# Optimization experiments

Measured on AMD Instinct MI355X. Metric: run time of the kernel, lower is better.

The kernel has to match this reference:

```python
import jax, jax.numpy as jnp
import numpy as np

B, T, D = 4, 2048, 1024
H = 16
DH = D // H
BASE = 10000.0


def _rope_tables(seq_len, dim):
    inv_freq = 1.0 / (BASE ** (np.arange(0, dim, 2, dtype=np.float32) / dim))
    pos = np.arange(seq_len, dtype=np.float32)
    freqs = np.outer(pos, inv_freq)            # (T, dim/2)
    emb = np.concatenate([freqs, freqs], -1)   # (T, dim)
    return jnp.asarray(np.cos(emb)), jnp.asarray(np.sin(emb))


def setup_inputs() -> dict:
    key = jax.random.key(0)
    ks = jax.random.split(key, 5)
    s = 1.0 / np.sqrt(D)
    x = jax.random.normal(ks[0], (B, T, D), jnp.float32)
    Wqkv = jax.random.normal(ks[1], (D, 3 * D), jnp.float32) * s
    bqkv = jnp.zeros((3 * D,), jnp.float32)
    Wproj = jax.random.normal(ks[2], (D, D), jnp.float32) * s
    bproj = jnp.zeros((D,), jnp.float32)
    cos, sin = _rope_tables(T, DH)
    return {"x": x, "Wqkv": Wqkv, "bqkv": bqkv, "Wproj": Wproj,
            "bproj": bproj, "cos": cos, "sin": sin}


def _rotate_half(u):
    u1, u2 = jnp.split(u, 2, axis=-1)
    return jnp.concatenate([-u2, u1], axis=-1)


def reference(x, Wqkv, bqkv, Wproj, bproj, cos, sin):
    b, t, d = x.shape
    qkv = x @ Wqkv + bqkv                       # (B, T, 3D)
    qkv = qkv.reshape(b, t, 3, H, DH)           # matches '(three h d)' order
    q, k, v = qkv[:, :, 0], qkv[:, :, 1], qkv[:, :, 2]  # (B, T, H, DH)
    c = cos[None, :, None, :]                   # (1, T, 1, DH)
    s = sin[None, :, None, :]
    q = q * c + _rotate_half(q) * s
    k = k * c + _rotate_half(k) * s
    scale = DH ** -0.5
    attn = jnp.einsum('bthd,bshd->bhts', q, k) * scale   # (B, H, T, T)
    attn = jax.nn.softmax(attn, axis=-1)
    out = jnp.einsum('bhts,bshd->bthd', attn, v)          # (B, T, H, DH)
    out = out.reshape(b, t, d)
    return out @ Wproj + bproj
```

## Files before the change

kernel.cpp:

```cpp
#include <hip/hip_runtime.h>


typedef _Float16 half_t;
typedef _Float16 half8 __attribute__((ext_vector_type(8)));
typedef _Float16 half4v __attribute__((ext_vector_type(4)));
typedef __fp16 fp16x2 __attribute__((ext_vector_type(2)));
typedef float floatx4 __attribute__((ext_vector_type(4)));

#define MFMA_F16 __builtin_amdgcn_mfma_f32_16x16x32_f16

constexpr int Bdim = 4, T = 2048, D = 1024, H = 16, DH = 64;
constexpr int Mrows = Bdim * T;
constexpr int N1 = 3 * D;
constexpr int KD = D;
constexpr int NT = KD / 32;

constexpr float QSCALE = 0.125f * 1.4426950408889634f;
constexpr float CSHIFT = 4.0f * 1.4426950408889634f;

__device__ __forceinline__ void gl_lds16(const half_t* g, half_t* l) {
  __builtin_amdgcn_global_load_lds(
      (const __attribute__((address_space(1))) void*)g,
      (__attribute__((address_space(3))) void*)l, 16, 0, 0);
}

__global__ __launch_bounds__(256) void cvt_kernel(const float* __restrict__ s,
                                                  half_t* __restrict__ d, int n4) {
  int i = blockIdx.x * 256 + threadIdx.x;
  if (i < n4) {
    float4 v = ((const float4*)s)[i];
    half4v h;
    h[0] = (half_t)v.x; h[1] = (half_t)v.y; h[2] = (half_t)v.z; h[3] = (half_t)v.w;
    ((half4v*)d)[i] = h;
  }
}

__global__ __launch_bounds__(64) void cvt_transpose(const float* __restrict__ W,
                                                    half_t* __restrict__ Wt,
                                                    int Kr, int Nc) {
  __shared__ half_t Th[32][36];
  const int l = threadIdx.x;
  const int n0 = blockIdx.x * 32, k0 = blockIdx.y * 32;
#pragma unroll
  for (int i = 0; i < 4; ++i) {
    int kk = (l >> 3) + i * 8;
    int nn4 = (l & 7) * 4;
    float4 v = *(const float4*)(W + (size_t)(k0 + kk) * Nc + n0 + nn4);
    half4v h;
    h[0] = (half_t)v.x; h[1] = (half_t)v.y; h[2] = (half_t)v.z; h[3] = (half_t)v.w;
    *(half4v*)&Th[kk][nn4] = h;
  }
  __syncthreads();
#pragma unroll
  for (int i = 0; i < 4; ++i) {
    int nn = (l >> 3) + i * 8;
    int kk4 = (l & 7) * 4;
    half4v h;
#pragma unroll
    for (int j = 0; j < 4; ++j) h[j] = Th[kk4 + j][nn];
    *(half4v*)(Wt + (size_t)(n0 + nn) * Kr + k0 + kk4) = h;
  }
}

__global__ __launch_bounds__(256, 3) void gemm_qkv_rope(
    const half_t* __restrict__ X, const half_t* __restrict__ Wt,
    const float* __restrict__ bias, const float* __restrict__ cosT,
    const float* __restrict__ sinT,
    half_t* __restrict__ Q, half_t* __restrict__ K, half_t* __restrict__ V) {
  __shared__ half_t As[3 * 128 * 32];
  __shared__ half_t Bs[3 * 128 * 32];
  const int tid = threadIdx.x;
  const int lane = tid & 63, wv = tid >> 6;
  const int wm = wv >> 1, wn = wv & 1;
  const int qd = lane >> 4, ln = lane & 15;
  const int flat = blockIdx.y * 24 + blockIdx.x;
  const int swzb = (flat & 7) * 192 + (flat >> 3);
  const int bn = swzb % 24, bm = swzb / 24;

  floatx4 acc[4][4] = {};

#pragma unroll
  for (int pt = 0; pt < 2; ++pt) {
#pragma unroll
    for (int p = 0; p < 2; ++p) {
      int c = tid + p * 256;
      int row = c >> 2, col = (c & 3) << 3;
      gl_lds16(X + (size_t)(bm * 128 + row) * KD + pt * 32 + col, As + pt * 4096 + c * 8);
      gl_lds16(Wt + (size_t)(bn * 128 + row) * KD + pt * 32 + col, Bs + pt * 4096 + c * 8);
    }
  }
  asm volatile("s_waitcnt vmcnt(4)" ::: "memory");
  __builtin_amdgcn_s_barrier();

  int rd = 0, st = 2;
  for (int t = 0; t < NT; ++t) {
    if (t + 2 < NT) {
#pragma unroll
      for (int p = 0; p < 2; ++p) {
        int c = tid + p * 256;
        int row = c >> 2, col = (c & 3) << 3;
        gl_lds16(X + (size_t)(bm * 128 + row) * KD + (t + 2) * 32 + col, As + st * 4096 + c * 8);
        gl_lds16(Wt + (size_t)(bn * 128 + row) * KD + (t + 2) * 32 + col, Bs + st * 4096 + c * 8);
      }
    }
    const half_t* Ab = As + rd * 4096;
    const half_t* Bb = Bs + rd * 4096;
    half8 af[4], bf[4];
#pragma unroll
    for (int mi = 0; mi < 4; ++mi)
      af[mi] = *(const half8*)&Ab[(wm * 64 + mi * 16 + ln) * 32 + qd * 8];
#pragma unroll
    for (int ni = 0; ni < 4; ++ni)
      bf[ni] = *(const half8*)&Bb[(wn * 64 + ni * 16 + ln) * 32 + qd * 8];
    __builtin_amdgcn_s_setprio(1);
#pragma unroll
    for (int mi = 0; mi < 4; ++mi)
#pragma unroll
      for (int ni = 0; ni < 4; ++ni)
        acc[mi][ni] = MFMA_F16(af[mi], bf[ni], acc[mi][ni], 0, 0, 0);
    __builtin_amdgcn_s_setprio(0);
    if (t + 2 < NT) asm volatile("s_waitcnt vmcnt(4)" ::: "memory");
    else            asm volatile("s_waitcnt vmcnt(0)" ::: "memory");
    __builtin_amdgcn_s_barrier();
    rd = (rd == 2) ? 0 : rd + 1;
    st = (st == 2) ? 0 : st + 1;
  }

  const int n0 = bn * 128 + wn * 64;
  const int sreg = n0 >> 10;
  const int h = (n0 & 1023) >> 6;
  float bv[4];
#pragma unroll
  for (int ni = 0; ni < 4; ++ni) bv[ni] = bias[n0 + ni * 16 + ln];

  if (sreg == 2) {
#pragma unroll
    for (int mi = 0; mi < 4; ++mi) {
      int m0 = bm * 128 + wm * 64 + mi * 16 + qd * 4;
      int b = m0 >> 11, t0 = m0 & (T - 1);
#pragma unroll
      for (int ni = 0; ni < 4; ++ni) {
        int dh = ni * 16 + ln;
        half4v hv;
#pragma unroll
        for (int r = 0; r < 4; ++r) hv[r] = (half_t)(acc[mi][ni][r] + bv[ni]);
        *(half4v*)(V + ((size_t)(b * H + h) * DH + dh) * T + t0) = hv;
      }
    }
  } else {
    const float qscale = (sreg == 0) ? QSCALE : 1.0f;
    half_t* OUT = (sreg == 0) ? Q : K;
#pragma unroll
    for (int mi = 0; mi < 4; ++mi) {
#pragma unroll
      for (int r = 0; r < 4; ++r) {
        int m = bm * 128 + wm * 64 + mi * 16 + qd * 4 + r;
        int b = m >> 11, t = m & (T - 1);
        float v0 = acc[mi][0][r] + bv[0];
        float v1 = acc[mi][1][r] + bv[1];
        float v2 = acc[mi][2][r] + bv[2];
        float v3 = acc[mi][3][r] + bv[3];
        float c0 = cosT[t * 64 + ln],      s0 = sinT[t * 64 + ln];
        float c1 = cosT[t * 64 + 16 + ln], s1 = sinT[t * 64 + 16 + ln];
        float c2 = cosT[t * 64 + 32 + ln], s2 = sinT[t * 64 + 32 + ln];
        float c3 = cosT[t * 64 + 48 + ln], s3 = sinT[t * 64 + 48 + ln];
        float o0 = v0 * c0 - v2 * s0;
        float o1 = v1 * c1 - v3 * s1;
        float o2 = v2 * c2 + v0 * s2;
        float o3 = v3 * c3 + v1 * s3;
        size_t base = ((size_t)(b * H + h) * T + t) * DH;
        OUT[base + 0 * 16 + ln] = (half_t)(o0 * qscale);
        OUT[base + 1 * 16 + ln] = (half_t)(o1 * qscale);
        OUT[base + 2 * 16 + ln] = (half_t)(o2 * qscale);
        OUT[base + 3 * 16 + ln] = (half_t)(o3 * qscale);
      }
    }
  }
}

__global__ __launch_bounds__(512, 4) void flash_attn(
    const half_t* __restrict__ Q, const half_t* __restrict__ K,
    const half_t* __restrict__ Vt, half_t* __restrict__ AO) {
  __shared__ __align__(16) half_t Klds[2][64 * 64];
  __shared__ __align__(16) half_t Vlds[2][64 * 64];
  __shared__ __align__(16) half_t Pw[8][32 * 64];
  const int tid = threadIdx.x;
  const int lane = tid & 63, wv = tid >> 6;
  const int qd = lane >> 4, ln = lane & 15;
  const int flat = blockIdx.y * 8 + blockIdx.x;
  const int swzb = (flat & 7) * 64 + (flat >> 3);
  const int bh = swzb >> 3;
  const int q0 = (swzb & 7) * 256 + wv * 32;
  const half_t* Qb = Q + (size_t)bh * T * DH;
  const half_t* Kb = K + (size_t)bh * T * DH;
  const half_t* Vb = Vt + (size_t)bh * DH * T;
  half_t* Pq = Pw[wv];
  const int swz = (ln & 7) << 3;
  const fp16x2 one2 = {(__fp16)1.0f, (__fp16)1.0f};

  const int sr = tid >> 3, sc8 = (tid & 7) << 3;
  const int stoff = sr * 64 + (sc8 ^ ((sr & 7) << 3));
  const half_t* Kg = Kb + (size_t)sr * DH + sc8;
  const half_t* Vg = Vb + (size_t)sr * T + sc8;

  half8 qf[2][2];
#pragma unroll
  for (int mi = 0; mi < 2; ++mi)
#pragma unroll
    for (int ks = 0; ks < 2; ++ks)
      qf[mi][ks] = *(const half8*)(Qb + (size_t)(q0 + mi * 16 + ln) * DH + ks * 32 + qd * 8);

  floatx4 Oacc[2][4] = {};
  float La[2] = {0.f, 0.f};
  float Lb2[2] = {0.f, 0.f};

  half8 kreg = *(const half8*)Kg;
  half8 vreg = *(const half8*)Vg;
  *(half8*)&Klds[0][stoff] = kreg;
  *(half8*)&Vlds[0][stoff] = vreg;
  kreg = *(const half8*)(Kg + (size_t)64 * DH);
  vreg = *(const half8*)(Vg + 64);

  for (int t = 0; t < T / 64; ++t) {
    __syncthreads();
    if (t + 1 < T / 64) {
      *(half8*)&Klds[(t + 1) & 1][stoff] = kreg;
      *(half8*)&Vlds[(t + 1) & 1][stoff] = vreg;
      if (t + 2 < T / 64) {
        kreg = *(const half8*)(Kg + (size_t)(t + 2) * 64 * DH);
        vreg = *(const half8*)(Vg + (t + 2) * 64);
      }
    }
    const half_t* Kc = Klds[t & 1];
    const half_t* Vc = Vlds[t & 1];

#pragma unroll
    for (int ni = 0; ni < 4; ++ni) {
      floatx4 s4[2] = {floatx4{-CSHIFT, -CSHIFT, -CSHIFT, -CSHIFT},
                       floatx4{-CSHIFT, -CSHIFT, -CSHIFT, -CSHIFT}};
#pragma unroll
      for (int ks = 0; ks < 2; ++ks) {
        int krow = ni * 16 + ln;
        half8 kf = *(const half8*)&Kc[krow * 64 + (((ks * 32) | (qd * 8)) ^ swz)];
        __builtin_amdgcn_s_setprio(1);
#pragma unroll
        for (int mi = 0; mi < 2; ++mi)
          s4[mi] = MFMA_F16(kf, qf[mi][ks], s4[mi], 0, 0, 0);
        __builtin_amdgcn_s_setprio(0);
      }
#pragma unroll
      for (int mi = 0; mi < 2; ++mi) {
        float p0 = __builtin_amdgcn_exp2f(s4[mi][0]);
        float p1 = __builtin_amdgcn_exp2f(s4[mi][1]);
        float p2 = __builtin_amdgcn_exp2f(s4[mi][2]);
        float p3 = __builtin_amdgcn_exp2f(s4[mi][3]);
        fp16x2 h01 = __builtin_amdgcn_cvt_pkrtz(p0, p1);
        fp16x2 h23 = __builtin_amdgcn_cvt_pkrtz(p2, p3);
        La[mi]  = __builtin_amdgcn_fdot2(h01, one2, La[mi], false);
        Lb2[mi] = __builtin_amdgcn_fdot2(h23, one2, Lb2[mi], false);
        union { half4v h4; fp16x2 h2[2]; } pu;
        pu.h2[0] = h01; pu.h2[1] = h23;
        int row = mi * 16 + ln;
        int chunk = ni * 16 + ((qd >> 1) << 3);
        int low = (qd & 1) << 2;
        *(half4v*)&Pq[row * 64 + (chunk ^ swz) + low] = pu.h4;
      }
    }

#pragma unroll
    for (int ks = 0; ks < 2; ++ks) {
      half8 pf[2];
#pragma unroll
      for (int mi = 0; mi < 2; ++mi)
        pf[mi] = *(const half8*)&Pq[(mi * 16 + ln) * 64 + (((ks * 32) | (qd * 8)) ^ swz)];
#pragma unroll
      for (int di = 0; di < 4; ++di) {
        half8 vf = *(const half8*)&Vc[(di * 16 + ln) * 64 + (((ks * 32) | (qd * 8)) ^ swz)];
        __builtin_amdgcn_s_setprio(1);
#pragma unroll
        for (int mi = 0; mi < 2; ++mi)
          Oacc[mi][di] = MFMA_F16(pf[mi], vf, Oacc[mi][di], 0, 0, 0);
        __builtin_amdgcn_s_setprio(0);
      }
    }
  }

  float Ls[2];
#pragma unroll
  for (int mi = 0; mi < 2; ++mi) {
    Ls[mi] = La[mi] + Lb2[mi];
    Ls[mi] += __shfl_xor(Ls[mi], 16);
    Ls[mi] += __shfl_xor(Ls[mi], 32);
  }

  const int b = bh >> 4, h = bh & 15;
#pragma unroll
  for (int mi = 0; mi < 2; ++mi) {
#pragma unroll
    for (int r = 0; r < 4; ++r) {
      float invL = 1.f / __shfl(Ls[mi], qd * 4 + r);
      int t = q0 + mi * 16 + qd * 4 + r;
      size_t base = ((size_t)b * T + t) * D + h * DH;
#pragma unroll
      for (int di = 0; di < 4; ++di)
        AO[base + di * 16 + ln] = (half_t)(Oacc[mi][di][r] * invL);
    }
  }
}

__global__ __launch_bounds__(256, 3) void gemm_proj(
    const half_t* __restrict__ X, const half_t* __restrict__ Wt,
    const float* __restrict__ bias, float* __restrict__ OUTF) {
  __shared__ half_t As[3 * 128 * 32];
  __shared__ half_t Bs[3 * 128 * 32];
  const int tid = threadIdx.x;
  const int lane = tid & 63, wv = tid >> 6;
  const int wm = wv >> 1, wn = wv & 1;
  const int qd = lane >> 4, ln = lane & 15;
  const int flat = blockIdx.y * 8 + blockIdx.x;
  const int swzb = (flat & 7) * 64 + (flat >> 3);
  const int bn = swzb % 8, bm = swzb / 8;

  floatx4 acc[4][4] = {};

#pragma unroll
  for (int pt = 0; pt < 2; ++pt) {
#pragma unroll
    for (int p = 0; p < 2; ++p) {
      int c = tid + p * 256;
      int row = c >> 2, col = (c & 3) << 3;
      gl_lds16(X + (size_t)(bm * 128 + row) * KD + pt * 32 + col, As + pt * 4096 + c * 8);
      gl_lds16(Wt + (size_t)(bn * 128 + row) * KD + pt * 32 + col, Bs + pt * 4096 + c * 8);
    }
  }
  asm volatile("s_waitcnt vmcnt(4)" ::: "memory");
  __builtin_amdgcn_s_barrier();

  int rd = 0, st = 2;
  for (int t = 0; t < NT; ++t) {
    if (t + 2 < NT) {
#pragma unroll
      for (int p = 0; p < 2; ++p) {
        int c = tid + p * 256;
        int row = c >> 2, col = (c & 3) << 3;
        gl_lds16(X + (size_t)(bm * 128 + row) * KD + (t + 2) * 32 + col, As + st * 4096 + c * 8);
        gl_lds16(Wt + (size_t)(bn * 128 + row) * KD + (t + 2) * 32 + col, Bs + st * 4096 + c * 8);
      }
    }
    const half_t* Ab = As + rd * 4096;
    const half_t* Bb = Bs + rd * 4096;
    half8 af[4], bf[4];
#pragma unroll
    for (int mi = 0; mi < 4; ++mi)
      af[mi] = *(const half8*)&Ab[(wm * 64 + mi * 16 + ln) * 32 + qd * 8];
#pragma unroll
    for (int ni = 0; ni < 4; ++ni)
      bf[ni] = *(const half8*)&Bb[(wn * 64 + ni * 16 + ln) * 32 + qd * 8];
    __builtin_amdgcn_s_setprio(1);
#pragma unroll
    for (int mi = 0; mi < 4; ++mi)
#pragma unroll
      for (int ni = 0; ni < 4; ++ni)
        acc[mi][ni] = MFMA_F16(af[mi], bf[ni], acc[mi][ni], 0, 0, 0);
    __builtin_amdgcn_s_setprio(0);
    if (t + 2 < NT) asm volatile("s_waitcnt vmcnt(4)" ::: "memory");
    else            asm volatile("s_waitcnt vmcnt(0)" ::: "memory");
    __builtin_amdgcn_s_barrier();
    rd = (rd == 2) ? 0 : rd + 1;
    st = (st == 2) ? 0 : st + 1;
  }

  const int n0 = bn * 128 + wn * 64;
  float bv[4];
#pragma unroll
  for (int ni = 0; ni < 4; ++ni) bv[ni] = bias[n0 + ni * 16 + ln];
#pragma unroll
  for (int mi = 0; mi < 4; ++mi) {
#pragma unroll
    for (int r = 0; r < 4; ++r) {
      int m = bm * 128 + wm * 64 + mi * 16 + qd * 4 + r;
#pragma unroll
      for (int ni = 0; ni < 4; ++ni)
        OUTF[(size_t)m * D + n0 + ni * 16 + ln] = acc[mi][ni][r] + bv[ni];
    }
  }
}

extern "C" void kernel_launch(void* const* d_in, const int* in_sizes, int n_in,
                              void* d_out, int out_size, void* d_ws, size_t ws_size,
                              hipStream_t stream) {
  const float* x     = (const float*)d_in[0];
  const float* Wqkv  = (const float*)d_in[1];
  const float* bqkv  = (const float*)d_in[2];
  const float* Wproj = (const float*)d_in[3];
  const float* bproj = (const float*)d_in[4];
  const float* cosT  = (const float*)d_in[5];
  const float* sinT  = (const float*)d_in[6];
  float* out = (float*)d_out;

  half_t* xh      = (half_t*)d_ws;
  half_t* Wqkvt   = xh + (size_t)Mrows * KD;
  half_t* Wprojt  = Wqkvt + (size_t)KD * N1;
  half_t* Qb      = Wprojt + (size_t)D * D;
  half_t* Kb      = Qb + (size_t)Bdim * H * T * DH;
  half_t* Vb      = Kb + (size_t)Bdim * H * T * DH;
  half_t* AO      = xh;

  cvt_kernel<<<(Mrows * KD / 4 + 255) / 256, 256, 0, stream>>>(x, xh, Mrows * KD / 4);
  cvt_transpose<<<dim3(N1 / 32, KD / 32), 64, 0, stream>>>(Wqkv, Wqkvt, KD, N1);
  cvt_transpose<<<dim3(D / 32, KD / 32), 64, 0, stream>>>(Wproj, Wprojt, KD, D);

  gemm_qkv_rope<<<dim3(N1 / 128, Mrows / 128), 256, 0, stream>>>(
      xh, Wqkvt, bqkv, cosT, sinT, Qb, Kb, Vb);
  flash_attn<<<dim3(T / 256, Bdim * H), 512, 0, stream>>>(Qb, Kb, Vb, AO);
  gemm_proj<<<dim3(D / 128, Mrows / 128), 256, 0, stream>>>(AO, Wprojt, bproj, out);
}
```

Measured before the change: 280.0 us.

## Fuse prep conversions into one kernel and deepen flash-attn K/V pipeline

```diff
diff --git a/kernel.cpp b/kernel.cpp
--- a/kernel.cpp
+++ b/kernel.cpp
@@ -24,23 +24,10 @@
       (__attribute__((address_space(3))) void*)l, 16, 0, 0);
 }
 
-__global__ __launch_bounds__(256) void cvt_kernel(const float* __restrict__ s,
-                                                  half_t* __restrict__ d, int n4) {
-  int i = blockIdx.x * 256 + threadIdx.x;
-  if (i < n4) {
-    float4 v = ((const float4*)s)[i];
-    half4v h;
-    h[0] = (half_t)v.x; h[1] = (half_t)v.y; h[2] = (half_t)v.z; h[3] = (half_t)v.w;
-    ((half4v*)d)[i] = h;
-  }
-}
-
-__global__ __launch_bounds__(64) void cvt_transpose(const float* __restrict__ W,
-                                                    half_t* __restrict__ Wt,
-                                                    int Kr, int Nc) {
-  __shared__ half_t Th[32][36];
-  const int l = threadIdx.x;
-  const int n0 = blockIdx.x * 32, k0 = blockIdx.y * 32;
+__device__ __forceinline__ void transpose_tile32(const float* __restrict__ W,
+                                                 half_t* __restrict__ Wt,
+                                                 int Kr, int Nc, int n0, int k0,
+                                                 int l, half_t (*Th)[36]) {
 #pragma unroll
   for (int i = 0; i < 4; ++i) {
     int kk = (l >> 3) + i * 8;
@@ -59,6 +46,29 @@
 #pragma unroll
     for (int j = 0; j < 4; ++j) h[j] = Th[kk4 + j][nn];
     *(half4v*)(Wt + (size_t)(n0 + nn) * Kr + k0 + kk4) = h;
+  }
+}
+
+__global__ __launch_bounds__(256) void prep_kernel(
+    const float* __restrict__ x, half_t* __restrict__ xh,
+    const float* __restrict__ Wqkv, half_t* __restrict__ Wqkvt,
+    const float* __restrict__ Wproj, half_t* __restrict__ Wprojt) {
+  __shared__ half_t Th[4][32][36];
+  const int bid = blockIdx.x, tid = threadIdx.x;
+  if (bid < 8192) {
+    int i = bid * 256 + tid;
+    float4 v = ((const float4*)x)[i];
+    half4v h;
+    h[0] = (half_t)v.x; h[1] = (half_t)v.y; h[2] = (half_t)v.z; h[3] = (half_t)v.w;
+    ((half4v*)xh)[i] = h;
+  } else if (bid < 8192 + 768) {
+    int tile = (bid - 8192) * 4 + (tid >> 6);
+    int n0 = (tile % 96) * 32, k0 = (tile / 96) * 32;
+    transpose_tile32(Wqkv, Wqkvt, KD, N1, n0, k0, tid & 63, Th[tid >> 6]);
+  } else {
+    int tile = (bid - 8960) * 4 + (tid >> 6);
+    int n0 = (tile % 32) * 32, k0 = (tile / 32) * 32;
+    transpose_tile32(Wproj, Wprojt, KD, D, n0, k0, tid & 63, Th[tid >> 6]);
   }
 }
 
@@ -181,9 +191,9 @@
 __global__ __launch_bounds__(512, 4) void flash_attn(
     const half_t* __restrict__ Q, const half_t* __restrict__ K,
     const half_t* __restrict__ Vt, half_t* __restrict__ AO) {
-  __shared__ __align__(16) half_t Klds[2][64 * 64];
-  __shared__ __align__(16) half_t Vlds[2][64 * 64];
-  __shared__ __align__(16) half_t Pw[8][32 * 64];
+  __shared__ __align__(16) half_t Klds[4][64 * 64];
+  __shared__ __align__(16) half_t Vlds[4][64 * 64];
+  __shared__ __align__(16) half_t Pw[8][32 * 32];
   const int tid = threadIdx.x;
   const int lane = tid & 63, wv = tid >> 6;
   const int qd = lane >> 4, ln = lane & 15;
@@ -196,6 +206,7 @@
   const half_t* Vb = Vt + (size_t)bh * DH * T;
   half_t* Pq = Pw[wv];
   const int swz = (ln & 7) << 3;
+  const int tau = (ln >> 1) & 3;
   const fp16x2 one2 = {(__fp16)1.0f, (__fp16)1.0f};
 
   const int sr = tid >> 3, sc8 = (tid & 7) << 3;
@@ -214,68 +225,71 @@
   float La[2] = {0.f, 0.f};
   float Lb2[2] = {0.f, 0.f};
 
-  half8 kreg = *(const half8*)Kg;
-  half8 vreg = *(const half8*)Vg;
-  *(half8*)&Klds[0][stoff] = kreg;
-  *(half8*)&Vlds[0][stoff] = vreg;
-  kreg = *(const half8*)(Kg + (size_t)64 * DH);
-  vreg = *(const half8*)(Vg + 64);
+  half8 k0r = *(const half8*)Kg;
+  half8 v0r = *(const half8*)Vg;
+  half8 k1r = *(const half8*)(Kg + (size_t)64 * DH);
+  half8 v1r = *(const half8*)(Vg + 64);
+  half8 kreg = *(const half8*)(Kg + (size_t)128 * DH);
+  half8 vreg = *(const half8*)(Vg + 128);
+  *(half8*)&Klds[0][stoff] = k0r;
+  *(half8*)&Vlds[0][stoff] = v0r;
+  *(half8*)&Klds[1][stoff] = k1r;
+  *(half8*)&Vlds[1][stoff] = v1r;
 
   for (int t = 0; t < T / 64; ++t) {
-    __syncthreads();
-    if (t + 1 < T / 64) {
-      *(half8*)&Klds[(t + 1) & 1][stoff] = kreg;
-      *(half8*)&Vlds[(t + 1) & 1][stoff] = vreg;
-      if (t + 2 < T / 64) {
-        kreg = *(const half8*)(Kg + (size_t)(t + 2) * 64 * DH);
-        vreg = *(const half8*)(Vg + (t + 2) * 64);
-      }
-    }
-    const half_t* Kc = Klds[t & 1];
-    const half_t* Vc = Vlds[t & 1];
-
-#pragma unroll
-    for (int ni = 0; ni < 4; ++ni) {
-      floatx4 s4[2] = {floatx4{-CSHIFT, -CSHIFT, -CSHIFT, -CSHIFT},
-                       floatx4{-CSHIFT, -CSHIFT, -CSHIFT, -CSHIFT}};
-#pragma unroll
-      for (int ks = 0; ks < 2; ++ks) {
-        int krow = ni * 16 + ln;
-        half8 kf = *(const half8*)&Kc[krow * 64 + (((ks * 32) | (qd * 8)) ^ swz)];
-        __builtin_amdgcn_s_setprio(1);
-#pragma unroll
-        for (int mi = 0; mi < 2; ++mi)
-          s4[mi] = MFMA_F16(kf, qf[mi][ks], s4[mi], 0, 0, 0);
-        __builtin_amdgcn_s_setprio(0);
-      }
-#pragma unroll
-      for (int mi = 0; mi < 2; ++mi) {
-        float p0 = __builtin_amdgcn_exp2f(s4[mi][0]);
-        float p1 = __builtin_amdgcn_exp2f(s4[mi][1]);
-        float p2 = __builtin_amdgcn_exp2f(s4[mi][2]);
-        float p3 = __builtin_amdgcn_exp2f(s4[mi][3]);
-        fp16x2 h01 = __builtin_amdgcn_cvt_pkrtz(p0, p1);
-        fp16x2 h23 = __builtin_amdgcn_cvt_pkrtz(p2, p3);
-        La[mi]  = __builtin_amdgcn_fdot2(h01, one2, La[mi], false);
-        Lb2[mi] = __builtin_amdgcn_fdot2(h23, one2, Lb2[mi], false);
-        union { half4v h4; fp16x2 h2[2]; } pu;
-        pu.h2[0] = h01; pu.h2[1] = h23;
-        int row = mi * 16 + ln;
-        int chunk = ni * 16 + ((qd >> 1) << 3);
-        int low = (qd & 1) << 2;
-        *(half4v*)&Pq[row * 64 + (chunk ^ swz) + low] = pu.h4;
-      }
-    }
-
-#pragma unroll
-    for (int ks = 0; ks < 2; ++ks) {
+    if ((t & 1) == 0) __syncthreads();
+    if (t + 2 < T / 64) {
+      *(half8*)&Klds[(t + 2) & 3][stoff] = kreg;
+      *(half8*)&Vlds[(t + 2) & 3][stoff] = vreg;
+      if (t + 3 < T / 64) {
+        kreg = *(const half8*)(Kg + (size_t)(t + 3) * 64 * DH);
+        vreg = *(const half8*)(Vg + (t + 3) * 64);
+      }
+    }
+    const half_t* Kc = Klds[t & 3];
+    const half_t* Vc = Vlds[t & 3];
+
+#pragma unroll
+    for (int ksh = 0; ksh < 2; ++ksh) {
+#pragma unroll
+      for (int nn = 0; nn < 2; ++nn) {
+        const int ni = ksh * 2 + nn;
+        floatx4 s4[2] = {floatx4{-CSHIFT, -CSHIFT, -CSHIFT, -CSHIFT},
+                         floatx4{-CSHIFT, -CSHIFT, -CSHIFT, -CSHIFT}};
+#pragma unroll
+        for (int ks = 0; ks < 2; ++ks) {
+          int krow = ni * 16 + ln;
+          half8 kf = *(const half8*)&Kc[krow * 64 + (((ks * 32) | (qd * 8)) ^ swz)];
+          __builtin_amdgcn_s_setprio(1);
+#pragma unroll
+          for (int mi = 0; mi < 2; ++mi)
+            s4[mi] = MFMA_F16(kf, qf[mi][ks], s4[mi], 0, 0, 0);
+          __builtin_amdgcn_s_setprio(0);
+        }
+#pragma unroll
+        for (int mi = 0; mi < 2; ++mi) {
+          float p0 = __builtin_amdgcn_exp2f(s4[mi][0]);
+          float p1 = __builtin_amdgcn_exp2f(s4[mi][1]);
+          float p2 = __builtin_amdgcn_exp2f(s4[mi][2]);
+          float p3 = __builtin_amdgcn_exp2f(s4[mi][3]);
+          fp16x2 h01 = __builtin_amdgcn_cvt_pkrtz(p0, p1);
+          fp16x2 h23 = __builtin_amdgcn_cvt_pkrtz(p2, p3);
+          La[mi]  = __builtin_amdgcn_fdot2(h01, one2, La[mi], false);
+          Lb2[mi] = __builtin_amdgcn_fdot2(h23, one2, Lb2[mi], false);
+          union { half4v h4; fp16x2 h2[2]; } pu;
+          pu.h2[0] = h01; pu.h2[1] = h23;
+          int row = mi * 16 + ln;
+          *(half4v*)&Pq[row * 32 + ((((nn * 4) + qd) ^ (tau << 1)) << 2)] = pu.h4;
+        }
+      }
+
       half8 pf[2];
 #pragma unroll
       for (int mi = 0; mi < 2; ++mi)
-        pf[mi] = *(const half8*)&Pq[(mi * 16 + ln) * 64 + (((ks * 32) | (qd * 8)) ^ swz)];
+        pf[mi] = *(const half8*)&Pq[(mi * 16 + ln) * 32 + ((qd ^ tau) << 3)];
 #pragma unroll
       for (int di = 0; di < 4; ++di) {
-        half8 vf = *(const half8*)&Vc[(di * 16 + ln) * 64 + (((ks * 32) | (qd * 8)) ^ swz)];
+        half8 vf = *(const half8*)&Vc[(di * 16 + ln) * 64 + (((ksh * 32) | (qd * 8)) ^ swz)];
         __builtin_amdgcn_s_setprio(1);
 #pragma unroll
         for (int mi = 0; mi < 2; ++mi)
@@ -406,9 +420,7 @@
   half_t* Vb      = Kb + (size_t)Bdim * H * T * DH;
   half_t* AO      = xh;
 
-  cvt_kernel<<<(Mrows * KD / 4 + 255) / 256, 256, 0, stream>>>(x, xh, Mrows * KD / 4);
-  cvt_transpose<<<dim3(N1 / 32, KD / 32), 64, 0, stream>>>(Wqkv, Wqkvt, KD, N1);
-  cvt_transpose<<<dim3(D / 32, KD / 32), 64, 0, stream>>>(Wproj, Wprojt, KD, D);
+  prep_kernel<<<9216, 256, 0, stream>>>(x, xh, Wqkv, Wqkvt, Wproj, Wprojt);
 
   gemm_qkv_rope<<<dim3(N1 / 128, Mrows / 128), 256, 0, stream>>>(
       xh, Wqkvt, bqkv, cosT, sinT, Qb, Kb, Vb);
```

Result: slower. 289.5 us (+3.4%).

## Halve attention block to 4 waves and interleave QK and PV per half tile

Applied to the files above, without the earlier changes.

```diff
diff --git a/kernel.cpp b/kernel.cpp
--- a/kernel.cpp
+++ b/kernel.cpp
@@ -178,30 +178,34 @@
   }
 }
 
-__global__ __launch_bounds__(512, 4) void flash_attn(
+__global__ __launch_bounds__(256, 4) void flash_attn(
     const half_t* __restrict__ Q, const half_t* __restrict__ K,
     const half_t* __restrict__ Vt, half_t* __restrict__ AO) {
   __shared__ __align__(16) half_t Klds[2][64 * 64];
   __shared__ __align__(16) half_t Vlds[2][64 * 64];
-  __shared__ __align__(16) half_t Pw[8][32 * 64];
+  __shared__ __align__(16) half_t Pw[4][32 * 32];
   const int tid = threadIdx.x;
   const int lane = tid & 63, wv = tid >> 6;
   const int qd = lane >> 4, ln = lane & 15;
-  const int flat = blockIdx.y * 8 + blockIdx.x;
-  const int swzb = (flat & 7) * 64 + (flat >> 3);
-  const int bh = swzb >> 3;
-  const int q0 = (swzb & 7) * 256 + wv * 32;
+  const int flat = blockIdx.y * 16 + blockIdx.x;
+  const int swzb = (flat & 7) * 128 + (flat >> 3);
+  const int bh = swzb >> 4;
+  const int q0 = (swzb & 15) * 128 + wv * 32;
   const half_t* Qb = Q + (size_t)bh * T * DH;
   const half_t* Kb = K + (size_t)bh * T * DH;
   const half_t* Vb = Vt + (size_t)bh * DH * T;
   half_t* Pq = Pw[wv];
   const int swz = (ln & 7) << 3;
+  const int tau = (ln >> 1) & 3;
   const fp16x2 one2 = {(__fp16)1.0f, (__fp16)1.0f};
 
-  const int sr = tid >> 3, sc8 = (tid & 7) << 3;
-  const int stoff = sr * 64 + (sc8 ^ ((sr & 7) << 3));
-  const half_t* Kg = Kb + (size_t)sr * DH + sc8;
-  const half_t* Vg = Vb + (size_t)sr * T + sc8;
+  int stoff[2], srr[2], sc8[2];
+#pragma unroll
+  for (int p = 0; p < 2; ++p) {
+    int c = tid + p * 256;
+    srr[p] = c >> 3; sc8[p] = (c & 7) << 3;
+    stoff[p] = srr[p] * 64 + (sc8[p] ^ ((srr[p] & 7) << 3));
+  }
 
   half8 qf[2][2];
 #pragma unroll
@@ -214,68 +218,83 @@
   float La[2] = {0.f, 0.f};
   float Lb2[2] = {0.f, 0.f};
 
-  half8 kreg = *(const half8*)Kg;
-  half8 vreg = *(const half8*)Vg;
-  *(half8*)&Klds[0][stoff] = kreg;
-  *(half8*)&Vlds[0][stoff] = vreg;
-  kreg = *(const half8*)(Kg + (size_t)64 * DH);
-  vreg = *(const half8*)(Vg + 64);
+  half8 kreg[2], vreg[2];
+#pragma unroll
+  for (int p = 0; p < 2; ++p) {
+    kreg[p] = *(const half8*)(Kb + (size_t)srr[p] * DH + sc8[p]);
+    vreg[p] = *(const half8*)(Vb + (size_t)srr[p] * T + sc8[p]);
+  }
+#pragma unroll
+  for (int p = 0; p < 2; ++p) {
+    *(half8*)&Klds[0][stoff[p]] = kreg[p];
+    *(half8*)&Vlds[0][stoff[p]] = vreg[p];
+  }
+#pragma unroll
+  for (int p = 0; p < 2; ++p) {
+    kreg[p] = *(const half8*)(Kb + (size_t)(64 + srr[p]) * DH + sc8[p]);
+    vreg[p] = *(const half8*)(Vb + (size_t)srr[p] * T + 64 + sc8[p]);
+  }
 
   for (int t = 0; t < T / 64; ++t) {
     __syncthreads();
     if (t + 1 < T / 64) {
-      *(half8*)&Klds[(t + 1) & 1][stoff] = kreg;
-      *(half8*)&Vlds[(t + 1) & 1][stoff] = vreg;
+#pragma unroll
+      for (int p = 0; p < 2; ++p) {
+        *(half8*)&Klds[(t + 1) & 1][stoff[p]] = kreg[p];
+        *(half8*)&Vlds[(t + 1) & 1][stoff[p]] = vreg[p];
+      }
       if (t + 2 < T / 64) {
-        kreg = *(const half8*)(Kg + (size_t)(t + 2) * 64 * DH);
-        vreg = *(const half8*)(Vg + (t + 2) * 64);
+#pragma unroll
+        for (int p = 0; p < 2; ++p) {
+          kreg[p] = *(const half8*)(Kb + (size_t)((t + 2) * 64 + srr[p]) * DH + sc8[p]);
+          vreg[p] = *(const half8*)(Vb + (size_t)srr[p] * T + (t + 2) * 64 + sc8[p]);
+        }
       }
     }
     const half_t* Kc = Klds[t & 1];
     const half_t* Vc = Vlds[t & 1];
 
 #pragma unroll
-    for (int ni = 0; ni < 4; ++ni) {
-      floatx4 s4[2] = {floatx4{-CSHIFT, -CSHIFT, -CSHIFT, -CSHIFT},
-                       floatx4{-CSHIFT, -CSHIFT, -CSHIFT, -CSHIFT}};
-#pragma unroll
-      for (int ks = 0; ks < 2; ++ks) {
-        int krow = ni * 16 + ln;
-        half8 kf = *(const half8*)&Kc[krow * 64 + (((ks * 32) | (qd * 8)) ^ swz)];
-        __builtin_amdgcn_s_setprio(1);
-#pragma unroll
-        for (int mi = 0; mi < 2; ++mi)
-          s4[mi] = MFMA_F16(kf, qf[mi][ks], s4[mi], 0, 0, 0);
-        __builtin_amdgcn_s_setprio(0);
-      }
-#pragma unroll
-      for (int mi = 0; mi < 2; ++mi) {
-        float p0 = __builtin_amdgcn_exp2f(s4[mi][0]);
-        float p1 = __builtin_amdgcn_exp2f(s4[mi][1]);
-        float p2 = __builtin_amdgcn_exp2f(s4[mi][2]);
-        float p3 = __builtin_amdgcn_exp2f(s4[mi][3]);
-        fp16x2 h01 = __builtin_amdgcn_cvt_pkrtz(p0, p1);
-        fp16x2 h23 = __builtin_amdgcn_cvt_pkrtz(p2, p3);
-        La[mi]  = __builtin_amdgcn_fdot2(h01, one2, La[mi], false);
-        Lb2[mi] = __builtin_amdgcn_fdot2(h23, one2, Lb2[mi], false);
-        union { half4v h4; fp16x2 h2[2]; } pu;
-        pu.h2[0] = h01; pu.h2[1] = h23;
-        int row = mi * 16 + ln;
-        int chunk = ni * 16 + ((qd >> 1) << 3);
-        int low = (qd & 1) << 2;
-        *(half4v*)&Pq[row * 64 + (chunk ^ swz) + low] = pu.h4;
-      }
-    }
-
-#pragma unroll
-    for (int ks = 0; ks < 2; ++ks) {
+    for (int ksh = 0; ksh < 2; ++ksh) {
+#pragma unroll
+      for (int nn = 0; nn < 2; ++nn) {
+        const int ni = ksh * 2 + nn;
+        floatx4 s4[2] = {floatx4{-CSHIFT, -CSHIFT, -CSHIFT, -CSHIFT},
+                         floatx4{-CSHIFT, -CSHIFT, -CSHIFT, -CSHIFT}};
+#pragma unroll
+        for (int ks = 0; ks < 2; ++ks) {
+          int krow = ni * 16 + ln;
+          half8 kf = *(const half8*)&Kc[krow * 64 + (((ks * 32) | (qd * 8)) ^ swz)];
+          __builtin_amdgcn_s_setprio(1);
+#pragma unroll
+          for (int mi = 0; mi < 2; ++mi)
+            s4[mi] = MFMA_F16(kf, qf[mi][ks], s4[mi], 0, 0, 0);
+          __builtin_amdgcn_s_setprio(0);
+        }
+#pragma unroll
+        for (int mi = 0; mi < 2; ++mi) {
+          float p0 = __builtin_amdgcn_exp2f(s4[mi][0]);
+          float p1 = __builtin_amdgcn_exp2f(s4[mi][1]);
+          float p2 = __builtin_amdgcn_exp2f(s4[mi][2]);
+          float p3 = __builtin_amdgcn_exp2f(s4[mi][3]);
+          fp16x2 h01 = __builtin_amdgcn_cvt_pkrtz(p0, p1);
+          fp16x2 h23 = __builtin_amdgcn_cvt_pkrtz(p2, p3);
+          La[mi]  = __builtin_amdgcn_fdot2(h01, one2, La[mi], false);
+          Lb2[mi] = __builtin_amdgcn_fdot2(h23, one2, Lb2[mi], false);
+          union { half4v h4; fp16x2 h2[2]; } pu;
+          pu.h2[0] = h01; pu.h2[1] = h23;
+          int row = mi * 16 + ln;
+          *(half4v*)&Pq[row * 32 + ((((nn * 4) + qd) ^ (tau << 1)) << 2)] = pu.h4;
+        }
+      }
+
       half8 pf[2];
 #pragma unroll
       for (int mi = 0; mi < 2; ++mi)
-        pf[mi] = *(const half8*)&Pq[(mi * 16 + ln) * 64 + (((ks * 32) | (qd * 8)) ^ swz)];
+        pf[mi] = *(const half8*)&Pq[(mi * 16 + ln) * 32 + ((qd ^ tau) << 3)];
 #pragma unroll
       for (int di = 0; di < 4; ++di) {
-        half8 vf = *(const half8*)&Vc[(di * 16 + ln) * 64 + (((ks * 32) | (qd * 8)) ^ swz)];
+        half8 vf = *(const half8*)&Vc[(di * 16 + ln) * 64 + (((ksh * 32) | (qd * 8)) ^ swz)];
         __builtin_amdgcn_s_setprio(1);
 #pragma unroll
         for (int mi = 0; mi < 2; ++mi)
@@ -412,6 +431,6 @@
 
   gemm_qkv_rope<<<dim3(N1 / 128, Mrows / 128), 256, 0, stream>>>(
       xh, Wqkvt, bqkv, cosT, sinT, Qb, Kb, Vb);
-  flash_attn<<<dim3(T / 256, Bdim * H), 512, 0, stream>>>(Qb, Kb, Vb, AO);
+  flash_attn<<<dim3(T / 128, Bdim * H), 256, 0, stream>>>(Qb, Kb, Vb, AO);
   gemm_proj<<<dim3(D / 128, Mrows / 128), 256, 0, stream>>>(AO, Wprojt, bproj, out);
 }
```

New measurement: 294.3 us. 1.05x slower.

## Use 256x128 GEMM tiles with BK=64, swizzled LDS and interleaved prefetch

Applied to the files above, without the earlier changes.

```diff
diff --git a/kernel.cpp b/kernel.cpp
--- a/kernel.cpp
+++ b/kernel.cpp
@@ -13,7 +13,7 @@
 constexpr int Mrows = Bdim * T;
 constexpr int N1 = 3 * D;
 constexpr int KD = D;
-constexpr int NT = KD / 32;
+constexpr int NT2 = KD / 64;
 
 constexpr float QSCALE = 0.125f * 1.4426950408889634f;
 constexpr float CSHIFT = 4.0f * 1.4426950408889634f;
@@ -62,69 +62,130 @@
   }
 }
 
-__global__ __launch_bounds__(256, 3) void gemm_qkv_rope(
+struct GemmFrags {
+  half8 af[4][2], bf[4][2];
+};
+
+#define GEMM8_BODY(X_, Wt_, BNBLK)                                              \
+  __shared__ half_t As[2][256 * 64];                                            \
+  __shared__ half_t Bs[2][128 * 64];                                            \
+  const int tid = threadIdx.x;                                                  \
+  const int lane = tid & 63, wv = tid >> 6;                                     \
+  const int wm = wv >> 1, wn = wv & 1;                                          \
+  const int qd = lane >> 4, ln = lane & 15;                                     \
+  const half_t* Asrc[4]; const half_t* Bsrc[2];                                 \
+  int destA[4], destB[2];                                                       \
+  _Pragma("unroll")                                                             \
+  for (int p = 0; p < 4; ++p) {                                                 \
+    int c = tid + p * 512, r = c >> 3, s = c & 7, g = s ^ (r & 7);              \
+    Asrc[p] = X_ + (size_t)(bm * 256 + r) * KD + g * 8;                         \
+    destA[p] = c * 8;                                                           \
+  }                                                                             \
+  _Pragma("unroll")                                                             \
+  for (int p = 0; p < 2; ++p) {                                                 \
+    int c = tid + p * 512, r = c >> 3, s = c & 7, g = s ^ (r & 7);              \
+    Bsrc[p] = Wt_ + (size_t)(bn * 128 + r) * KD + g * 8;                        \
+    destB[p] = c * 8;                                                           \
+  }                                                                             \
+  int offA[4][2], offB[4][2];                                                   \
+  _Pragma("unroll")                                                             \
+  for (int mi = 0; mi < 4; ++mi) {                                              \
+    int r = wm * 64 + mi * 16 + ln;                                             \
+    _Pragma("unroll")                                                           \
+    for (int ks = 0; ks < 2; ++ks)                                              \
+      offA[mi][ks] = r * 64 + (((ks * 4 + qd) ^ (r & 7)) << 3);                 \
+  }                                                                             \
+  _Pragma("unroll")                                                             \
+  for (int ni = 0; ni < 4; ++ni) {                                              \
+    int r = wn * 64 + ni * 16 + ln;                                             \
+    _Pragma("unroll")                                                           \
+    for (int ks = 0; ks < 2; ++ks)                                              \
+      offB[ni][ks] = r * 64 + (((ks * 4 + qd) ^ (r & 7)) << 3);                 \
+  }                                                                             \
+  floatx4 acc[4][4] = {};                                                       \
+  _Pragma("unroll")                                                             \
+  for (int t0 = 0; t0 < 2; ++t0) {                                              \
+    _Pragma("unroll")                                                           \
+    for (int p = 0; p < 4; ++p) gl_lds16(Asrc[p] + t0 * 64, &As[t0][0] + destA[p]); \
+    _Pragma("unroll")                                                           \
+    for (int p = 0; p < 2; ++p) gl_lds16(Bsrc[p] + t0 * 64, &Bs[t0][0] + destB[p]); \
+  }                                                                             \
+  asm volatile("s_waitcnt vmcnt(6)" ::: "memory");                              \
+  __builtin_amdgcn_s_barrier();                                                 \
+  for (int t = 0; t < NT2; ++t) {                                               \
+    const int bsel = t & 1;                                                     \
+    const half_t* Ab = &As[bsel][0];                                            \
+    const half_t* Bb = &Bs[bsel][0];                                            \
+    half_t* An = &As[bsel][0];                                                  \
+    half_t* Bn = &Bs[bsel][0];                                                  \
+    const bool st = (t + 2 < NT2);                                              \
+    GemmFrags f;                                                                \
+    _Pragma("unroll")                                                           \
+    for (int mi = 0; mi < 4; ++mi)                                              \
+      _Pragma("unroll")                                                         \
+      for (int ks = 0; ks < 2; ++ks) f.af[mi][ks] = *(const half8*)&Ab[offA[mi][ks]]; \
+    _Pragma("unroll")                                                           \
+    for (int ni = 0; ni < 4; ++ni)                                              \
+      _Pragma("unroll")                                                         \
+      for (int ks = 0; ks < 2; ++ks) f.bf[ni][ks] = *(const half8*)&Bb[offB[ni][ks]]; \
+    asm volatile("s_waitcnt lgkmcnt(0)" ::: "memory");                          \
+    __builtin_amdgcn_sched_barrier(0);                                          \
+    __builtin_amdgcn_s_barrier();                                               \
+    __builtin_amdgcn_s_setprio(1);                                              \
+    _Pragma("unroll")                                                           \
+    for (int mi = 0; mi < 2; ++mi)                                              \
+      _Pragma("unroll")                                                         \
+      for (int ni = 0; ni < 4; ++ni)                                            \
+        acc[mi][ni] = MFMA_F16(f.af[mi][0], f.bf[ni][0], acc[mi][ni], 0, 0, 0); \
+    __builtin_amdgcn_s_setprio(0);                                              \
+    __builtin_amdgcn_s_barrier();                                               \
+    if (st) { gl_lds16(Asrc[0] + (t + 2) * 64, An + destA[0]);                  \
+              gl_lds16(Asrc[1] + (t + 2) * 64, An + destA[1]); }                \
+    __builtin_amdgcn_s_barrier();                                               \
+    __builtin_amdgcn_s_setprio(1);                                              \
+    _Pragma("unroll")                                                           \
+    for (int mi = 2; mi < 4; ++mi)                                              \
+      _Pragma("unroll")                                                         \
+      for (int ni = 0; ni < 4; ++ni)                                            \
+        acc[mi][ni] = MFMA_F16(f.af[mi][0], f.bf[ni][0], acc[mi][ni], 0, 0, 0); \
+    __builtin_amdgcn_s_setprio(0);                                              \
+    __builtin_amdgcn_s_barrier();                                               \
+    if (st) { gl_lds16(Asrc[2] + (t + 2) * 64, An + destA[2]);                  \
+              gl_lds16(Asrc[3] + (t + 2) * 64, An + destA[3]); }                \
+    __builtin_amdgcn_s_barrier();                                               \
+    __builtin_amdgcn_s_setprio(1);                                              \
+    _Pragma("unroll")                                                           \
+    for (int mi = 0; mi < 2; ++mi)                                              \
+      _Pragma("unroll")                                                         \
+      for (int ni = 0; ni < 4; ++ni)                                            \
+        acc[mi][ni] = MFMA_F16(f.af[mi][1], f.bf[ni][1], acc[mi][ni], 0, 0, 0); \
+    __builtin_amdgcn_s_setprio(0);                                              \
+    __builtin_amdgcn_s_barrier();                                               \
+    if (st) { gl_lds16(Bsrc[0] + (t + 2) * 64, Bn + destB[0]);                  \
+              gl_lds16(Bsrc[1] + (t + 2) * 64, Bn + destB[1]); }                \
+    __builtin_amdgcn_s_barrier();                                               \
+    __builtin_amdgcn_s_setprio(1);                                              \
+    _Pragma("unroll")                                                           \
+    for (int mi = 2; mi < 4; ++mi)                                              \
+      _Pragma("unroll")                                                         \
+      for (int ni = 0; ni < 4; ++ni)                                            \
+        acc[mi][ni] = MFMA_F16(f.af[mi][1], f.bf[ni][1], acc[mi][ni], 0, 0, 0); \
+    __builtin_amdgcn_s_setprio(0);                                              \
+    if (st) asm volatile("s_waitcnt vmcnt(6)" ::: "memory");                    \
+    else    asm volatile("s_waitcnt vmcnt(0)" ::: "memory");                    \
+    __builtin_amdgcn_s_barrier();                                               \
+  }
+
+__global__ __launch_bounds__(512, 1) void gemm_qkv_rope(
     const half_t* __restrict__ X, const half_t* __restrict__ Wt,
     const float* __restrict__ bias, const float* __restrict__ cosT,
     const float* __restrict__ sinT,
     half_t* __restrict__ Q, half_t* __restrict__ K, half_t* __restrict__ V) {
-  __shared__ half_t As[3 * 128 * 32];
-  __shared__ half_t Bs[3 * 128 * 32];
-  const int tid = threadIdx.x;
-  const int lane = tid & 63, wv = tid >> 6;
-  const int wm = wv >> 1, wn = wv & 1;
-  const int qd = lane >> 4, ln = lane & 15;
   const int flat = blockIdx.y * 24 + blockIdx.x;
-  const int swzb = (flat & 7) * 192 + (flat >> 3);
+  const int swzb = (flat & 7) * 96 + (flat >> 3);
   const int bn = swzb % 24, bm = swzb / 24;
 
-  floatx4 acc[4][4] = {};
-
-#pragma unroll
-  for (int pt = 0; pt < 2; ++pt) {
-#pragma unroll
-    for (int p = 0; p < 2; ++p) {
-      int c = tid + p * 256;
-      int row = c >> 2, col = (c & 3) << 3;
-      gl_lds16(X + (size_t)(bm * 128 + row) * KD + pt * 32 + col, As + pt * 4096 + c * 8);
-      gl_lds16(Wt + (size_t)(bn * 128 + row) * KD + pt * 32 + col, Bs + pt * 4096 + c * 8);
-    }
-  }
-  asm volatile("s_waitcnt vmcnt(4)" ::: "memory");
-  __builtin_amdgcn_s_barrier();
-
-  int rd = 0, st = 2;
-  for (int t = 0; t < NT; ++t) {
-    if (t + 2 < NT) {
-#pragma unroll
-      for (int p = 0; p < 2; ++p) {
-        int c = tid + p * 256;
-        int row = c >> 2, col = (c & 3) << 3;
-        gl_lds16(X + (size_t)(bm * 128 + row) * KD + (t + 2) * 32 + col, As + st * 4096 + c * 8);
-        gl_lds16(Wt + (size_t)(bn * 128 + row) * KD + (t + 2) * 32 + col, Bs + st * 4096 + c * 8);
-      }
-    }
-    const half_t* Ab = As + rd * 4096;
-    const half_t* Bb = Bs + rd * 4096;
-    half8 af[4], bf[4];
-#pragma unroll
-    for (int mi = 0; mi < 4; ++mi)
-      af[mi] = *(const half8*)&Ab[(wm * 64 + mi * 16 + ln) * 32 + qd * 8];
-#pragma unroll
-    for (int ni = 0; ni < 4; ++ni)
-      bf[ni] = *(const half8*)&Bb[(wn * 64 + ni * 16 + ln) * 32 + qd * 8];
-    __builtin_amdgcn_s_setprio(1);
-#pragma unroll
-    for (int mi = 0; mi < 4; ++mi)
-#pragma unroll
-      for (int ni = 0; ni < 4; ++ni)
-        acc[mi][ni] = MFMA_F16(af[mi], bf[ni], acc[mi][ni], 0, 0, 0);
-    __builtin_amdgcn_s_setprio(0);
-    if (t + 2 < NT) asm volatile("s_waitcnt vmcnt(4)" ::: "memory");
-    else            asm volatile("s_waitcnt vmcnt(0)" ::: "memory");
-    __builtin_amdgcn_s_barrier();
-    rd = (rd == 2) ? 0 : rd + 1;
-    st = (st == 2) ? 0 : st + 1;
-  }
+  GEMM8_BODY(X, Wt, 24)
 
   const int n0 = bn * 128 + wn * 64;
   const int sreg = n0 >> 10;
@@ -136,7 +197,7 @@
   if (sreg == 2) {
 #pragma unroll
     for (int mi = 0; mi < 4; ++mi) {
-      int m0 = bm * 128 + wm * 64 + mi * 16 + qd * 4;
+      int m0 = bm * 256 + wm * 64 + mi * 16 + qd * 4;
       int b = m0 >> 11, t0 = m0 & (T - 1);
 #pragma unroll
       for (int ni = 0; ni < 4; ++ni) {
@@ -154,7 +215,7 @@
     for (int mi = 0; mi < 4; ++mi) {
 #pragma unroll
       for (int r = 0; r < 4; ++r) {
-        int m = bm * 128 + wm * 64 + mi * 16 + qd * 4 + r;
+        int m = bm * 256 + wm * 64 + mi * 16 + qd * 4 + r;
         int b = m >> 11, t = m & (T - 1);
         float v0 = acc[mi][0][r] + bv[0];
         float v1 = acc[mi][1][r] + bv[1];
@@ -174,6 +235,31 @@
         OUT[base + 2 * 16 + ln] = (half_t)(o2 * qscale);
         OUT[base + 3 * 16 + ln] = (half_t)(o3 * qscale);
       }
+    }
+  }
+}
+
+__global__ __launch_bounds__(512, 1) void gemm_proj(
+    const half_t* __restrict__ X, const half_t* __restrict__ Wt,
+    const float* __restrict__ bias, float* __restrict__ OUTF) {
+  const int flat = blockIdx.y * 8 + blockIdx.x;
+  const int swzb = (flat & 7) * 32 + (flat >> 3);
+  const int bn = swzb % 8, bm = swzb / 8;
+
+  GEMM8_BODY(X, Wt, 8)
+
+  const int n0 = bn * 128 + wn * 64;
+  float bv[4];
+#pragma unroll
+  for (int ni = 0; ni < 4; ++ni) bv[ni] = bias[n0 + ni * 16 + ln];
+#pragma unroll
+  for (int mi = 0; mi < 4; ++mi) {
+#pragma unroll
+    for (int r = 0; r < 4; ++r) {
+      int m = bm * 256 + wm * 64 + mi * 16 + qd * 4 + r;
+#pragma unroll
+      for (int ni = 0; ni < 4; ++ni)
+        OUTF[(size_t)m * D + n0 + ni * 16 + ln] = acc[mi][ni][r] + bv[ni];
     }
   }
 }
@@ -308,84 +394,6 @@
   }
 }
 
-__global__ __launch_bounds__(256, 3) void gemm_proj(
-    const half_t* __restrict__ X, const half_t* __restrict__ Wt,
-    const float* __restrict__ bias, float* __restrict__ OUTF) {
-  __shared__ half_t As[3 * 128 * 32];
-  __shared__ half_t Bs[3 * 128 * 32];
-  const int tid = threadIdx.x;
-  const int lane = tid & 63, wv = tid >> 6;
-  const int wm = wv >> 1, wn = wv & 1;
-  const int qd = lane >> 4, ln = lane & 15;
-  const int flat = blockIdx.y * 8 + blockIdx.x;
-  const int swzb = (flat & 7) * 64 + (flat >> 3);
-  const int bn = swzb % 8, bm = swzb / 8;
-
-  floatx4 acc[4][4] = {};
-
-#pragma unroll
-  for (int pt = 0; pt < 2; ++pt) {
-#pragma unroll
-    for (int p = 0; p < 2; ++p) {
-      int c = tid + p * 256;
-      int row = c >> 2, col = (c & 3) << 3;
-      gl_lds16(X + (size_t)(bm * 128 + row) * KD + pt * 32 + col, As + pt * 4096 + c * 8);
-      gl_lds16(Wt + (size_t)(bn * 128 + row) * KD + pt * 32 + col, Bs + pt * 4096 + c * 8);
-    }
-  }
-  asm volatile("s_waitcnt vmcnt(4)" ::: "memory");
-  __builtin_amdgcn_s_barrier();
-
-  int rd = 0, st = 2;
-  for (int t = 0; t < NT; ++t) {
-    if (t + 2 < NT) {
-#pragma unroll
-      for (int p = 0; p < 2; ++p) {
-        int c = tid + p * 256;
-        int row = c >> 2, col = (c & 3) << 3;
-        gl_lds16(X + (size_t)(bm * 128 + row) * KD + (t + 2) * 32 + col, As + st * 4096 + c * 8);
-        gl_lds16(Wt + (size_t)(bn * 128 + row) * KD + (t + 2) * 32 + col, Bs + st * 4096 + c * 8);
-      }
-    }
-    const half_t* Ab = As + rd * 4096;
-    const half_t* Bb = Bs + rd * 4096;
-    half8 af[4], bf[4];
-#pragma unroll
-    for (int mi = 0; mi < 4; ++mi)
-      af[mi] = *(const half8*)&Ab[(wm * 64 + mi * 16 + ln) * 32 + qd * 8];
-#pragma unroll
-    for (int ni = 0; ni < 4; ++ni)
-      bf[ni] = *(const half8*)&Bb[(wn * 64 + ni * 16 + ln) * 32 + qd * 8];
-    __builtin_amdgcn_s_setprio(1);
-#pragma unroll
-    for (int mi = 0; mi < 4; ++mi)
-#pragma unroll
-      for (int ni = 0; ni < 4; ++ni)
-        acc[mi][ni] = MFMA_F16(af[mi], bf[ni], acc[mi][ni], 0, 0, 0);
-    __builtin_amdgcn_s_setprio(0);
-    if (t + 2 < NT) asm volatile("s_waitcnt vmcnt(4)" ::: "memory");
-    else            asm volatile("s_waitcnt vmcnt(0)" ::: "memory");
-    __builtin_amdgcn_s_barrier();
-    rd = (rd == 2) ? 0 : rd + 1;
-    st = (st == 2) ? 0 : st + 1;
-  }
-
-  const int n0 = bn * 128 + wn * 64;
-  float bv[4];
-#pragma unroll
-  for (int ni = 0; ni < 4; ++ni) bv[ni] = bias[n0 + ni * 16 + ln];
-#pragma unroll
-  for (int mi = 0; mi < 4; ++mi) {
-#pragma unroll
-    for (int r = 0; r < 4; ++r) {
-      int m = bm * 128 + wm * 64 + mi * 16 + qd * 4 + r;
-#pragma unroll
-      for (int ni = 0; ni < 4; ++ni)
-        OUTF[(size_t)m * D + n0 + ni * 16 + ln] = acc[mi][ni][r] + bv[ni];
-    }
-  }
-}
-
 extern "C" void kernel_launch(void* const* d_in, const int* in_sizes, int n_in,
                               void* d_out, int out_size, void* d_ws, size_t ws_size,
                               hipStream_t stream) {
@@ -410,8 +418,8 @@
   cvt_transpose<<<dim3(N1 / 32, KD / 32), 64, 0, stream>>>(Wqkv, Wqkvt, KD, N1);
   cvt_transpose<<<dim3(D / 32, KD / 32), 64, 0, stream>>>(Wproj, Wprojt, KD, D);
 
-  gemm_qkv_rope<<<dim3(N1 / 128, Mrows / 128), 256, 0, stream>>>(
+  gemm_qkv_rope<<<dim3(N1 / 128, Mrows / 256), 512, 0, stream>>>(
       xh, Wqkvt, bqkv, cosT, sinT, Qb, Kb, Vb);
   flash_attn<<<dim3(T / 256, Bdim * H), 512, 0, stream>>>(Qb, Kb, Vb, AO);
-  gemm_proj<<<dim3(D / 128, Mrows / 128), 256, 0, stream>>>(AO, Wprojt, bproj, out);
-}
+  gemm_proj<<<dim3(D / 128, Mrows / 256), 512, 0, stream>>>(AO, Wprojt, bproj, out);
+}
```

Measured after the change: 287.0 us. +2.5%, slower.
